# Kernel optimization log

Measured on AMD Instinct MI355X. Metric: run time of the kernel, lower is better.

The kernel has to match this reference:

```python
import jax, jax.numpy as jnp
import numpy as np

_EPS = 1e-7
N_POINTS = 16384
N_FRAMES = 10


def setup_inputs() -> dict:
    key = jax.random.key(0)
    k1, k2, k3, k4 = jax.random.split(key, 4)
    points = jax.random.normal(k1, (N_POINTS, 3), dtype=jnp.float32)
    time_indice = jax.random.randint(k2, (N_POINTS,), 0, N_FRAMES)
    est_poses = jax.random.normal(k3, (N_FRAMES, 4, 4), dtype=jnp.float32)
    gt_poses = jax.random.normal(k4, (N_FRAMES, 4, 4), dtype=jnp.float32)
    return {"points": points, "time_indice": time_indice,
            "est_poses": est_poses, "gt_poses": gt_poses}


def _align_frames(points, time_indice, poses):
    # Vectorized form of the per-frame masked loop: every point's time index
    # lies in [0, n_frames), so gathering its pose is equivalent.
    P = poses[time_indice]                      # [N,4,4]
    R = P[:, :3, :3]                            # [N,3,3]
    t = P[:, :3, 3]                             # [N,3]
    return jnp.einsum('nij,nj->ni', R, points) + t


def reference(points, time_indice, est_poses, gt_poses):
    est_points = _align_frames(points, time_indice, est_poses)  # [N,3]
    gt_points = _align_frames(points, time_indice, gt_poses)    # [N,3]

    # weights: 1 on points of frame 1, normalized
    w = (time_indice == 1).astype(points.dtype)
    w = w / (w.sum() + _EPS)

    # Chamfer distance: squared pairwise distances gt -> est (brute force)
    gt_sq = jnp.sum(gt_points * gt_points, axis=1)   # [N]
    est_sq = jnp.sum(est_points * est_points, axis=1)  # [N]
    d2 = gt_sq[:, None] + est_sq[None, :] - 2.0 * (gt_points @ est_points.T)  # [N,N]
    dist1 = jnp.min(d2, axis=1)  # per gt point, nearest est
    dist2 = jnp.min(d2, axis=0)  # per est point, nearest gt
    chamfer = ((dist1 * w).sum() + (dist2 * w).sum()) * 0.5

    # weighted L2 distance
    l2 = (jnp.linalg.norm(est_points - gt_points, axis=1) * w).sum()
    return chamfer, l2
```

## Files before the change

kernel.cpp:

```cpp
#include <hip/hip_runtime.h>
#include <math.h>

#define N_PTS   16384
#define EPS     1e-7f
#define JSPLIT  8
#define JSLICE  (N_PTS / JSPLIT)
#define NBLK    256
#define NTHR    1024
#define NWAVE   (NTHR / 64)
#define MAXACT  2048
#define PPW     8

__device__ unsigned g_partial[2 * JSPLIT * MAXACT];
__device__ int      g_done = 0;

__global__ __launch_bounds__(NTHR) void fused_kernel(
        const float* __restrict__ pts, const int* __restrict__ ti,
        const float* __restrict__ est_poses, const float* __restrict__ gt_poses,
        float* __restrict__ out) {
    const int t    = threadIdx.x;
    const int lane = t & 63;
    const int w    = t >> 6;
    const int side = blockIdx.x >> 7;
    const int s    = (blockIdx.x >> 4) & 7;
    const int bsub = blockIdx.x & 15;

    __shared__ int    s_cnt[256];
    __shared__ int    s_glist[MAXACT];
    __shared__ float4 s_q[JSLICE];
    __shared__ float  s_red[NTHR];
    __shared__ int    s_nact;
    __shared__ int    s_lastflag;

    int vals[16];
    #pragma unroll
    for (int i = 0; i < 16; ++i)
        vals[i] = ti[(w * 16 + i) * 64 + lane];
    #pragma unroll
    for (int i = 0; i < 16; ++i) {
        unsigned long long mask = __ballot(vals[i] == 1);
        if (lane == 0) s_cnt[w * 16 + i] = __popcll(mask);
    }
    __syncthreads();
    int ocnt = (t < 256) ? s_cnt[t] : 0;
    for (int d = 1; d < 256; d <<= 1) {
        int v = (t < 256 && t >= d) ? s_cnt[t - d] : 0;
        __syncthreads();
        if (t < 256) s_cnt[t] += v;
        __syncthreads();
    }
    if (t == 255) s_nact = s_cnt[255];
    if (t < 256) s_cnt[t] -= ocnt;
    __syncthreads();
    const int nact = min(s_nact, MAXACT);
    #pragma unroll
    for (int i = 0; i < 16; ++i) {
        int c = w * 16 + i;
        unsigned long long mask = __ballot(vals[i] == 1);
        if (vals[i] == 1) {
            int rank = __popcll(mask & ((1ull << lane) - 1ull));
            int pos  = s_cnt[c] + rank;
            if (pos < MAXACT) s_glist[pos] = c * 64 + lane;
        }
    }

    const float* qposes = side ? gt_poses : est_poses;
    for (int r = t; r < JSLICE; r += NTHR) {
        int j = s * JSLICE + r;
        float px = pts[3 * j], py = pts[3 * j + 1], pz = pts[3 * j + 2];
        const float* M = qposes + ti[j] * 16;
        float x = M[0] * px + M[1] * py + M[2]  * pz + M[3];
        float y = M[4] * px + M[5] * py + M[6]  * pz + M[7];
        float z = M[8] * px + M[9] * py + M[10] * pz + M[11];
        s_q[r] = make_float4(x, y, z, x * x + y * y + z * z);
    }
    __syncthreads();

    const int g     = bsub * NWAVE + w;
    const int gbase = g * PPW;
    if (gbase < nact) {
        const float* PM = (side ? est_poses : gt_poses) + 16;
        float p2x[PPW], p2y[PPW], p2z[PPW], pw[PPW], m[PPW];
        #pragma unroll
        for (int k = 0; k < PPW; ++k) {
            int pos = gbase + k;
            if (pos >= nact) pos = nact - 1;
            int idx = s_glist[pos];
            float px = pts[3 * idx], py = pts[3 * idx + 1], pz = pts[3 * idx + 2];
            float x = PM[0] * px + PM[1] * py + PM[2]  * pz + PM[3];
            float y = PM[4] * px + PM[5] * py + PM[6]  * pz + PM[7];
            float z = PM[8] * px + PM[9] * py + PM[10] * pz + PM[11];
            p2x[k] = -2.0f * x; p2y[k] = -2.0f * y; p2z[k] = -2.0f * z;
            pw[k]  = x * x + y * y + z * z;
            m[k]   = 3.4e38f;
        }
        for (int jj = 0; jj < JSLICE; jj += 128) {
            float4 q0 = s_q[jj + lane];
            float4 q1 = s_q[jj + 64 + lane];
            #pragma unroll
            for (int k = 0; k < PPW; ++k) {
                float e0 = fmaf(p2x[k], q0.x,
                           fmaf(p2y[k], q0.y, fmaf(p2z[k], q0.z, q0.w)));
                float e1 = fmaf(p2x[k], q1.x,
                           fmaf(p2y[k], q1.y, fmaf(p2z[k], q1.z, q1.w)));
                m[k] = fminf(m[k], fminf(e0, e1));
            }
        }
        #pragma unroll
        for (int k = 0; k < PPW; ++k) {
            #pragma unroll
            for (int o = 32; o > 0; o >>= 1)
                m[k] = fminf(m[k], __shfl_xor(m[k], o));
        }
        if (lane == 0) {
            #pragma unroll
            for (int k = 0; k < PPW; ++k) {
                int pos = gbase + k;
                if (pos < nact)
                    g_partial[(side * JSPLIT + s) * MAXACT + pos] =
                        __float_as_uint(pw[k] + m[k]);
            }
        }
    }

    __syncthreads();
    if (t == 0) {
        __threadfence();
        s_lastflag = (atomicAdd(&g_done, 1) == NBLK - 1);
    }
    __syncthreads();
    if (!s_lastflag) return;

    float msum = 0.0f;
    for (int a = t; a < 2 * nact; a += NTHR) {
        int aside = a >= nact;
        int pos   = aside ? a - nact : a;
        unsigned base = (unsigned)(aside * JSPLIT) * MAXACT + pos;
        float mn = 3.4e38f;
        #pragma unroll
        for (int ss = 0; ss < JSPLIT; ++ss) {
            unsigned u = atomicAdd(&g_partial[base + ss * MAXACT], 0u);
            mn = fminf(mn, __uint_as_float(u));
        }
        msum += mn;
    }
    float l2s = 0.0f;
    const float* PE1 = est_poses + 16;
    const float* PG1 = gt_poses + 16;
    for (int a = t; a < nact; a += NTHR) {
        int idx = s_glist[a];
        float px = pts[3 * idx], py = pts[3 * idx + 1], pz = pts[3 * idx + 2];
        float ex = PE1[0] * px + PE1[1] * py + PE1[2]  * pz + PE1[3];
        float ey = PE1[4] * px + PE1[5] * py + PE1[6]  * pz + PE1[7];
        float ez = PE1[8] * px + PE1[9] * py + PE1[10] * pz + PE1[11];
        float gx = PG1[0] * px + PG1[1] * py + PG1[2]  * pz + PG1[3];
        float gy = PG1[4] * px + PG1[5] * py + PG1[6]  * pz + PG1[7];
        float gz = PG1[8] * px + PG1[9] * py + PG1[10] * pz + PG1[11];
        float dx = ex - gx, dy = ey - gy, dz = ez - gz;
        l2s += sqrtf(dx * dx + dy * dy + dz * dz);
    }
    s_red[t] = msum;
    __syncthreads();
    for (int d = NTHR / 2; d > 0; d >>= 1) {
        if (t < d) s_red[t] += s_red[t + d];
        __syncthreads();
    }
    float chamfer_raw = s_red[0];
    __syncthreads();
    s_red[t] = l2s;
    __syncthreads();
    for (int d = NTHR / 2; d > 0; d >>= 1) {
        if (t < d) s_red[t] += s_red[t + d];
        __syncthreads();
    }
    if (t == 0) {
        float inv = 1.0f / ((float)nact + EPS);
        out[0] = 0.5f * chamfer_raw * inv;
        out[1] = s_red[0] * inv;
        g_done = 0;
    }
}

extern "C" void kernel_launch(void* const* d_in, const int* in_sizes, int n_in,
                              void* d_out, int out_size, void* d_ws, size_t ws_size,
                              hipStream_t stream) {
    const float* pts       = (const float*)d_in[0];
    const int*   ti        = (const int*)d_in[1];
    const float* est_poses = (const float*)d_in[2];
    const float* gt_poses  = (const float*)d_in[3];
    float* out = (float*)d_out;

    fused_kernel<<<NBLK, NTHR, 0, stream>>>(pts, ti, est_poses, gt_poses, out);
}
```

Before: 28.81 us.

## Pack FMAs into 2-wide vectors, atomicMax min-keys, wave-level prefix scan

```diff
diff --git a/kernel.cpp b/kernel.cpp
--- a/kernel.cpp
+++ b/kernel.cpp
@@ -11,8 +11,21 @@
 #define MAXACT  2048
 #define PPW     8
 
-__device__ unsigned g_partial[2 * JSPLIT * MAXACT];
+typedef float v2f __attribute__((ext_vector_type(2)));
+
+__device__ unsigned g_minkey[2 * MAXACT];
 __device__ int      g_done = 0;
+
+__device__ inline unsigned ikey(float f) {
+    unsigned b = __float_as_uint(f);
+    unsigned fk = (b & 0x80000000u) ? ~b : (b | 0x80000000u);
+    return ~fk;
+}
+__device__ inline float idec(unsigned k) {
+    unsigned fk = ~k;
+    unsigned b = (fk & 0x80000000u) ? (fk ^ 0x80000000u) : ~fk;
+    return __uint_as_float(b);
+}
 
 __global__ __launch_bounds__(NTHR) void fused_kernel(
         const float* __restrict__ pts, const int* __restrict__ ti,
@@ -42,15 +55,24 @@
         if (lane == 0) s_cnt[w * 16 + i] = __popcll(mask);
     }
     __syncthreads();
-    int ocnt = (t < 256) ? s_cnt[t] : 0;
-    for (int d = 1; d < 256; d <<= 1) {
-        int v = (t < 256 && t >= d) ? s_cnt[t - d] : 0;
-        __syncthreads();
-        if (t < 256) s_cnt[t] += v;
-        __syncthreads();
-    }
-    if (t == 255) s_nact = s_cnt[255];
-    if (t < 256) s_cnt[t] -= ocnt;
+    if (w == 0) {
+        int c[4];
+        #pragma unroll
+        for (int i = 0; i < 4; ++i) c[i] = s_cnt[lane * 4 + i];
+        int tot = c[0] + c[1] + c[2] + c[3];
+        int x = tot;
+        #pragma unroll
+        for (int o = 1; o < 64; o <<= 1) {
+            int y = __shfl_up(x, o);
+            if (lane >= o) x += y;
+        }
+        int excl = x - tot;
+        s_cnt[lane * 4 + 0] = excl;
+        s_cnt[lane * 4 + 1] = excl + c[0];
+        s_cnt[lane * 4 + 2] = excl + c[0] + c[1];
+        s_cnt[lane * 4 + 3] = excl + c[0] + c[1] + c[2];
+        if (lane == 63) s_nact = x;
+    }
     __syncthreads();
     const int nact = min(s_nact, MAXACT);
     #pragma unroll
@@ -80,45 +102,63 @@
     const int gbase = g * PPW;
     if (gbase < nact) {
         const float* PM = (side ? est_poses : gt_poses) + 16;
-        float p2x[PPW], p2y[PPW], p2z[PPW], pw[PPW], m[PPW];
-        #pragma unroll
-        for (int k = 0; k < PPW; ++k) {
-            int pos = gbase + k;
-            if (pos >= nact) pos = nact - 1;
-            int idx = s_glist[pos];
-            float px = pts[3 * idx], py = pts[3 * idx + 1], pz = pts[3 * idx + 2];
-            float x = PM[0] * px + PM[1] * py + PM[2]  * pz + PM[3];
-            float y = PM[4] * px + PM[5] * py + PM[6]  * pz + PM[7];
-            float z = PM[8] * px + PM[9] * py + PM[10] * pz + PM[11];
-            p2x[k] = -2.0f * x; p2y[k] = -2.0f * y; p2z[k] = -2.0f * z;
-            pw[k]  = x * x + y * y + z * z;
-            m[k]   = 3.4e38f;
-        }
+        v2f p2x[4], p2y[4], p2z[4], pw2[4], macc[4];
+        #pragma unroll
+        for (int kp = 0; kp < 4; ++kp) {
+            float xx[2], yy[2], zz[2], ww[2];
+            #pragma unroll
+            for (int h = 0; h < 2; ++h) {
+                int pos = gbase + 2 * kp + h;
+                if (pos >= nact) pos = nact - 1;
+                int idx = s_glist[pos];
+                float px = pts[3 * idx], py = pts[3 * idx + 1], pz = pts[3 * idx + 2];
+                float x = PM[0] * px + PM[1] * py + PM[2]  * pz + PM[3];
+                float y = PM[4] * px + PM[5] * py + PM[6]  * pz + PM[7];
+                float z = PM[8] * px + PM[9] * py + PM[10] * pz + PM[11];
+                xx[h] = x; yy[h] = y; zz[h] = z;
+                ww[h] = x * x + y * y + z * z;
+            }
+            p2x[kp] = (v2f){-2.0f * xx[0], -2.0f * xx[1]};
+            p2y[kp] = (v2f){-2.0f * yy[0], -2.0f * yy[1]};
+            p2z[kp] = (v2f){-2.0f * zz[0], -2.0f * zz[1]};
+            pw2[kp] = (v2f){ww[0], ww[1]};
+            macc[kp] = (v2f){3.4e38f, 3.4e38f};
+        }
+
         for (int jj = 0; jj < JSLICE; jj += 128) {
             float4 q0 = s_q[jj + lane];
             float4 q1 = s_q[jj + 64 + lane];
             #pragma unroll
-            for (int k = 0; k < PPW; ++k) {
-                float e0 = fmaf(p2x[k], q0.x,
-                           fmaf(p2y[k], q0.y, fmaf(p2z[k], q0.z, q0.w)));
-                float e1 = fmaf(p2x[k], q1.x,
-                           fmaf(p2y[k], q1.y, fmaf(p2z[k], q1.z, q1.w)));
-                m[k] = fminf(m[k], fminf(e0, e1));
+            for (int kp = 0; kp < 4; ++kp) {
+                v2f e0 = p2x[kp] * q0.x + (p2y[kp] * q0.y + (p2z[kp] * q0.z + q0.w));
+                v2f e1 = p2x[kp] * q1.x + (p2y[kp] * q1.y + (p2z[kp] * q1.z + q1.w));
+                macc[kp].x = fminf(macc[kp].x, fminf(e0.x, e1.x));
+                macc[kp].y = fminf(macc[kp].y, fminf(e0.y, e1.y));
             }
         }
+
+        float mm[PPW];
+        #pragma unroll
+        for (int kp = 0; kp < 4; ++kp) {
+            mm[2 * kp]     = macc[kp].x;
+            mm[2 * kp + 1] = macc[kp].y;
+        }
         #pragma unroll
         for (int k = 0; k < PPW; ++k) {
             #pragma unroll
             for (int o = 32; o > 0; o >>= 1)
-                m[k] = fminf(m[k], __shfl_xor(m[k], o));
+                mm[k] = fminf(mm[k], __shfl_xor(mm[k], o));
         }
         if (lane == 0) {
             #pragma unroll
-            for (int k = 0; k < PPW; ++k) {
-                int pos = gbase + k;
-                if (pos < nact)
-                    g_partial[(side * JSPLIT + s) * MAXACT + pos] =
-                        __float_as_uint(pw[k] + m[k]);
+            for (int kp = 0; kp < 4; ++kp) {
+                int pos0 = gbase + 2 * kp;
+                if (pos0 < nact)
+                    atomicMax(&g_minkey[side * MAXACT + pos0],
+                              ikey(pw2[kp].x + mm[2 * kp]));
+                if (pos0 + 1 < nact)
+                    atomicMax(&g_minkey[side * MAXACT + pos0 + 1],
+                              ikey(pw2[kp].y + mm[2 * kp + 1]));
             }
         }
     }
@@ -134,15 +174,9 @@
     float msum = 0.0f;
     for (int a = t; a < 2 * nact; a += NTHR) {
         int aside = a >= nact;
-        int pos   = aside ? a - nact : a;
-        unsigned base = (unsigned)(aside * JSPLIT) * MAXACT + pos;
-        float mn = 3.4e38f;
-        #pragma unroll
-        for (int ss = 0; ss < JSPLIT; ++ss) {
-            unsigned u = atomicAdd(&g_partial[base + ss * MAXACT], 0u);
-            mn = fminf(mn, __uint_as_float(u));
-        }
-        msum += mn;
+        int pos   = a - aside * nact;
+        unsigned k = atomicExch(&g_minkey[aside * MAXACT + pos], 0u);
+        msum += idec(k);
     }
     float l2s = 0.0f;
     const float* PE1 = est_poses + 16;
@@ -177,7 +211,7 @@
         float inv = 1.0f / ((float)nact + EPS);
         out[0] = 0.5f * chamfer_raw * inv;
         out[1] = s_red[0] * inv;
-        g_done = 0;
+        atomicExch(&g_done, 0);
     }
 }
 
```

Measured after the change: 26.40 us. 1.09x faster.
